# Kernel optimization log

Measured on AMD Instinct MI355X. Metric: run time of the kernel, lower is better.

Reference implementation:

```python
import jax, jax.numpy as jnp
import numpy as np
import math

EMBED_DIM = 1024
N_HEADS = 16
HEAD_DIM = EMBED_DIM // N_HEADS
NUM_FEATURES = 32
R_NODES = 2
EPS = 1e-06
C_CONST = 2.0 + EPS
CHUNK = 512


def setup_inputs() -> dict:
    key = jax.random.key(0)
    ks = jax.random.split(key, 8)
    B, T = 2, 4096
    x = jax.random.normal(ks[0], (B, T, EMBED_DIM), dtype=jnp.float32)
    w_qkv = jax.random.normal(ks[1], (3 * EMBED_DIM, EMBED_DIM), dtype=jnp.float32) * 0.02
    b_qkv = jnp.zeros((3 * EMBED_DIM,), dtype=jnp.float32)
    w_out = jax.random.normal(ks[2], (EMBED_DIM, EMBED_DIM), dtype=jnp.float32) * 0.02
    b_out = jnp.zeros((EMBED_DIM,), dtype=jnp.float32)
    omega = jax.random.normal(ks[3], (R_NODES, N_HEADS, HEAD_DIM, NUM_FEATURES), dtype=jnp.float32)
    nodes, weights = np.polynomial.laguerre.laggauss(R_NODES)
    quad_nodes = jnp.asarray(nodes, dtype=jnp.float32) / C_CONST
    quad_weights = jnp.asarray(weights, dtype=jnp.float32) / C_CONST
    return {"x": x, "w_qkv": w_qkv, "b_qkv": b_qkv, "w_out": w_out,
            "b_out": b_out, "omega": omega, "quad_nodes": quad_nodes,
            "quad_weights": quad_weights}


def _compute_features(z, omega, quad_nodes, quad_weights):
    # z: [B,H,T,D] -> fused features [B,H,T,R*M]
    R, M = omega.shape[0], omega.shape[-1]
    nrm = jnp.linalg.norm(z, axis=-1, keepdims=True)
    zn = z / jnp.maximum(nrm, 1e-12)  # F.normalize
    proj = jnp.einsum('bhtd,rhdm->rbhtm', zn, omega)
    inv_sqrt_m = 1.0 / math.sqrt(M)
    poly = (proj ** 2) * inv_sqrt_m
    s = quad_nodes.reshape(R, 1, 1, 1, 1)
    sqrt_2s = jnp.sqrt(2.0 * jnp.maximum(quad_nodes, 0.0)).reshape(R, 1, 1, 1, 1)
    exp_arg = jnp.clip(proj * sqrt_2s - s, -20.0, 20.0)
    prf = jnp.exp(exp_arg) * inv_sqrt_m
    sqw = jnp.sqrt(jnp.maximum(quad_weights, 0.0)).reshape(R, 1, 1, 1, 1)
    fused = poly * prf * sqw  # [R,B,H,T,M]
    B, H, T = z.shape[0], z.shape[1], z.shape[2]
    return jnp.transpose(fused, (1, 2, 3, 0, 4)).reshape(B, H, T, R * M)


def _forward(x, w_qkv, b_qkv, w_out, b_out, omega, quad_nodes, quad_weights):
    B, T, C = x.shape
    H, D = N_HEADS, HEAD_DIM
    qkv = x @ w_qkv.T + b_qkv  # [B,T,3C]
    q, k, v = jnp.split(qkv, 3, axis=-1)
    def to_bhtd(t):
        return jnp.transpose(t.reshape(B, T, H, D), (0, 2, 1, 3)).astype(jnp.float32)
    q, k, v = to_bhtd(q), to_bhtd(k), to_bhtd(v)
    qf = _compute_features(q, omega, quad_nodes, quad_weights)  # [B,H,T,F]
    kf = _compute_features(k, omega, quad_nodes, quad_weights)
    F_dim = qf.shape[-1]
    nc = T // CHUNK
    # chunked causal linear attention via scan over chunks
    def to_chunks(t):  # [B,H,T,...] -> [nc,B,H,CHUNK,...]
        new_shape = (t.shape[0], t.shape[1], nc, CHUNK) + t.shape[3:]
        return jnp.moveaxis(t.reshape(new_shape), 2, 0)
    qf_c, kf_c, v_c = to_chunks(qf), to_chunks(kf), to_chunks(v)

    kv0 = jnp.zeros((B, H, F_dim, D), dtype=jnp.float32)
    k0 = jnp.zeros((B, H, F_dim), dtype=jnp.float32)

    def step(carry, inp):
        kv_s, k_s = carry
        qc, kc, vc = inp
        kv_prod = jnp.einsum('bhtf,bhtd->bhtfd', kc, vc)
        kv_cum = jnp.cumsum(kv_prod, axis=2) + kv_s[:, :, None]
        k_cum = jnp.cumsum(kc, axis=2) + k_s[:, :, None]
        ctx = jnp.einsum('bhtf,bhtfd->bhtd', qc, kv_cum)
        den = jnp.maximum(jnp.einsum('bhtf,bhtf->bht', qc, k_cum), 1e-06)
        out_c = ctx / den[..., None]
        return (kv_cum[:, :, -1], k_cum[:, :, -1]), out_c

    _, out_chunks = jax.lax.scan(step, (kv0, k0), (qf_c, kf_c, v_c))
    out = jnp.moveaxis(out_chunks, 0, 2).reshape(B, H, T, D)  # [B,H,T,D]
    out = jnp.transpose(out, (0, 2, 1, 3)).reshape(B, T, C)
    return out @ w_out.T + b_out


def reference(x, w_qkv, b_qkv, w_out, b_out, omega, quad_nodes, quad_weights):
    return _forward(x, w_qkv, b_qkv, w_out, b_out, omega, quad_nodes, quad_weights)
```

## Files before the change

kernel.cpp:

```cpp
#include <hip/hip_runtime.h>
#include <math.h>

#define EMBED   1024
#define THREEC  3072
#define NH      16
#define HD      64
#define NFEAT   64
#define RN      2
#define MM_     32
#define B_      2
#define T_      4096
#define L_      64
#define NC_     64
#define BH_     32

typedef __attribute__((ext_vector_type(8))) short bf16x8;
typedef __attribute__((ext_vector_type(4))) float f32x4;

__device__ __forceinline__ float bf2f(short s) {
    unsigned u = ((unsigned)(unsigned short)s) << 16;
    return __builtin_bit_cast(float, u);
}
__device__ __forceinline__ short f2bf(float f) {
    unsigned u = __builtin_bit_cast(unsigned, f);
    u += 0x7fff + ((u >> 16) & 1);
    return (short)(u >> 16);
}
__device__ __forceinline__ void gload16(const short* g, short* l) {
    __builtin_amdgcn_global_load_lds(
        (const __attribute__((address_space(1))) void*)g,
        (__attribute__((address_space(3))) void*)l, 16, 0, 0);
}

__global__ __launch_bounds__(256) void cast_kernel(
    const float* __restrict__ in, short* __restrict__ out, int n8)
{
    int i = blockIdx.x * 256 + threadIdx.x;
    if (i >= n8) return;
    const float4* p = (const float4*)in + (size_t)i * 2;
    float4 a = p[0], b = p[1];
    bf16x8 o = { f2bf(a.x), f2bf(a.y), f2bf(a.z), f2bf(a.w),
                 f2bf(b.x), f2bf(b.y), f2bf(b.z), f2bf(b.w) };
    *((bf16x8*)out + i) = o;
}

__global__ __launch_bounds__(256) void omega_prep(
    const float* __restrict__ omega, short* __restrict__ hi, short* __restrict__ lo)
{
    int i = blockIdx.x * 256 + threadIdx.x;
    if (i >= NH * NFEAT * HD) return;
    int d = i & 63;
    int f = (i >> 6) & 63;
    int h = i >> 12;
    int r = f >> 5, m = f & 31;
    float w = omega[(((size_t)(r * NH + h) * HD + d) * MM_) + m];
    short a = f2bf(w);
    hi[i] = a;
    lo[i] = f2bf(w - bf2f(a));
}

template<int OUTBF>
__global__ __launch_bounds__(256) void gemm_bf16(
    const short* __restrict__ A,
    const short* __restrict__ W,
    const float* __restrict__ bias,
    float* __restrict__ Cf, short* __restrict__ Cb,
    int M, int N, int K)
{
    __shared__ short lA[2][128 * 32];
    __shared__ short lB[2][128 * 32];
    const int tid  = threadIdx.x;
    const int bm   = blockIdx.y * 128;
    const int bn   = blockIdx.x * 128;
    const int lane = tid & 63;
    const int wave = tid >> 6;
    const int row0 = (wave >> 1) * 64;
    const int col0 = (wave & 1) * 64;
    const int lr   = lane & 15;
    const int kg8  = (lane >> 4) * 8;

    f32x4 acc[4][4] = {};

#define STAGE(buf, k0)                                                        \
    {                                                                         \
        _Pragma("unroll")                                                     \
        for (int i = 0; i < 2; ++i) {                                         \
            int idx = i * 256 + tid;                                          \
            int row = idx >> 2, kq = (idx & 3) * 8;                           \
            gload16(&A[(size_t)(bm + row) * K + (k0) + kq], &lA[buf][idx * 8]); \
            gload16(&W[(size_t)(bn + row) * K + (k0) + kq], &lB[buf][idx * 8]); \
        }                                                                     \
    }

    const int KT = K >> 5;
    STAGE(0, 0);
    __syncthreads();
    int cur = 0;
    for (int kt = 0; kt < KT; ++kt) {
        if (kt + 1 < KT) STAGE(cur ^ 1, (kt + 1) * 32);
        const short* As = lA[cur];
        const short* Bs = lB[cur];
        bf16x8 af[4], bfr[4];
        #pragma unroll
        for (int m = 0; m < 4; ++m)
            af[m] = *(const bf16x8*)&As[(row0 + m * 16 + lr) * 32 + kg8];
        #pragma unroll
        for (int n = 0; n < 4; ++n)
            bfr[n] = *(const bf16x8*)&Bs[(col0 + n * 16 + lr) * 32 + kg8];
        #pragma unroll
        for (int m = 0; m < 4; ++m)
            #pragma unroll
            for (int n = 0; n < 4; ++n)
                acc[m][n] = __builtin_amdgcn_mfma_f32_16x16x32_bf16(
                    af[m], bfr[n], acc[m][n], 0, 0, 0);
        __syncthreads();
        cur ^= 1;
    }
#undef STAGE

    #pragma unroll
    for (int n = 0; n < 4; ++n) {
        const int col = bn + col0 + n * 16 + (lane & 15);
        const float bv = bias[col];
        #pragma unroll
        for (int m = 0; m < 4; ++m) {
            const int rbase = bm + row0 + m * 16 + (lane >> 4) * 4;
            #pragma unroll
            for (int j = 0; j < 4; ++j) {
                const float v = acc[m][n][j] + bv;
                if (OUTBF) Cb[(size_t)(rbase + j) * N + col] = f2bf(v);
                else       Cf[(size_t)(rbase + j) * N + col] = v;
            }
        }
    }
}

__global__ __launch_bounds__(256) void features_mfma(
    const short* __restrict__ qkvb,
    const short* __restrict__ omgH,
    const short* __restrict__ omgL,
    const float* __restrict__ qn,
    const float* __restrict__ qw,
    short* __restrict__ qf,
    short* __restrict__ kf)
{
    __shared__ short zq[64][72];
    __shared__ short zk[64][72];
    __shared__ short omh[64][72];
    __shared__ short oml[64][72];
    __shared__ float invn[2][64];

    const int tid = threadIdx.x;
    const int bh  = blockIdx.x >> 6;
    const int tb  = blockIdx.x & 63;
    const int b   = bh >> 4, h = bh & 15;
    const int t0  = tb * 64;

    {
        const int row = tid >> 2;
        const int c0  = (tid & 3) * 16;
        const size_t zbase = ((size_t)(b * T_ + t0 + row)) * THREEC + h * HD + c0;
        const size_t obase = ((size_t)h * NFEAT + row) * HD + c0;
        *(bf16x8*)&zq[row][c0]      = *(const bf16x8*)&qkvb[zbase];
        *(bf16x8*)&zq[row][c0 + 8]  = *(const bf16x8*)&qkvb[zbase + 8];
        *(bf16x8*)&zk[row][c0]      = *(const bf16x8*)&qkvb[zbase + EMBED];
        *(bf16x8*)&zk[row][c0 + 8]  = *(const bf16x8*)&qkvb[zbase + EMBED + 8];
        *(bf16x8*)&omh[row][c0]     = *(const bf16x8*)&omgH[obase];
        *(bf16x8*)&omh[row][c0 + 8] = *(const bf16x8*)&omgH[obase + 8];
        *(bf16x8*)&oml[row][c0]     = *(const bf16x8*)&omgL[obase];
        *(bf16x8*)&oml[row][c0 + 8] = *(const bf16x8*)&omgL[obase + 8];
    }
    __syncthreads();

    {
        const int t = tid >> 2;
        const int q = tid & 3;
        #pragma unroll
        for (int p = 0; p < 2; ++p) {
            const short* Z = p ? &zk[t][q * 16] : &zq[t][q * 16];
            float ss = 0.0f;
            #pragma unroll
            for (int j = 0; j < 16; ++j) { float v = bf2f(Z[j]); ss += v * v; }
            ss += __shfl_xor(ss, 1, 64);
            ss += __shfl_xor(ss, 2, 64);
            if (q == 0) invn[p][t] = 1.0f / fmaxf(sqrtf(ss), 1e-12f);
        }
    }
    __syncthreads();

    const int wave = tid >> 6;
    const int lane = tid & 63;
    const int p    = wave >> 1;
    const int half = wave & 1;
    const short (*Z)[72] = p ? zk : zq;

    const float s0 = qn[0], s1 = qn[1];
    const float sq2s0 = sqrtf(2.0f * fmaxf(s0, 0.0f));
    const float sq2s1 = sqrtf(2.0f * fmaxf(s1, 0.0f));
    const float sc0 = sqrtf(fmaxf(qw[0], 0.0f)) * (1.0f / 32.0f);
    const float sc1 = sqrtf(fmaxf(qw[1], 0.0f)) * (1.0f / 32.0f);

    const int lr  = lane & 15;
    const int kg8 = (lane >> 4) * 8;

    f32x4 acc[2][4] = {};
    #pragma unroll
    for (int kk = 0; kk < 2; ++kk) {
        bf16x8 a[2], bh8[4], bl8[4];
        #pragma unroll
        for (int m = 0; m < 2; ++m)
            a[m] = *(const bf16x8*)&Z[half * 32 + m * 16 + lr][kk * 32 + kg8];
        #pragma unroll
        for (int n = 0; n < 4; ++n) {
            bh8[n] = *(const bf16x8*)&omh[n * 16 + lr][kk * 32 + kg8];
            bl8[n] = *(const bf16x8*)&oml[n * 16 + lr][kk * 32 + kg8];
        }
        #pragma unroll
        for (int m = 0; m < 2; ++m)
            #pragma unroll
            for (int n = 0; n < 4; ++n) {
                acc[m][n] = __builtin_amdgcn_mfma_f32_16x16x32_bf16(
                    a[m], bh8[n], acc[m][n], 0, 0, 0);
                acc[m][n] = __builtin_amdgcn_mfma_f32_16x16x32_bf16(
                    a[m], bl8[n], acc[m][n], 0, 0, 0);
            }
    }

    short* dstbase = (p ? kf : qf) + ((size_t)bh * T_ + t0) * NFEAT;
    #pragma unroll
    for (int n = 0; n < 4; ++n) {
        const int f = n * 16 + (lane & 15);
        const float s_r   = (n < 2) ? s0 : s1;
        const float sq2s  = (n < 2) ? sq2s0 : sq2s1;
        const float scale = (n < 2) ? sc0 : sc1;
        #pragma unroll
        for (int m = 0; m < 2; ++m) {
            const int tb4 = half * 32 + m * 16 + (lane >> 4) * 4;
            #pragma unroll
            for (int j = 0; j < 4; ++j) {
                const int t = tb4 + j;
                const float proj = acc[m][n][j] * invn[p][t];
                const float arg = fminf(fmaxf(proj * sq2s - s_r, -20.0f), 20.0f);
                const float val = proj * proj * __expf(arg) * scale;
                dstbase[(size_t)t * NFEAT + f] = f2bf(val);
            }
        }
    }
}

__global__ __launch_bounds__(256) void chunk_sums(
    const short* __restrict__ kf,
    const short* __restrict__ qkvb,
    float* __restrict__ cKV,
    float* __restrict__ cK)
{
    __shared__ float kfs[64][64];
    __shared__ float vs[64][64];
    float (*st)[65] = (float(*)[65])kfs;

    const int tid = threadIdx.x;
    const int chunk = blockIdx.x;
    const int bh = chunk >> 6, c = chunk & 63;
    const int b = bh >> 4, h = bh & 15;
    const int t0 = c * L_;

    {
        const int row = tid >> 2;
        const int c0  = (tid & 3) * 16;
        const short* krow = kf + ((size_t)bh * T_ + t0 + row) * NFEAT;
        const short* vrow = qkvb + ((size_t)(b * T_ + t0 + row)) * THREEC + 2 * EMBED + h * HD;
        bf16x8 k0 = *(const bf16x8*)&krow[c0], k1 = *(const bf16x8*)&krow[c0 + 8];
        bf16x8 v0 = *(const bf16x8*)&vrow[c0], v1 = *(const bf16x8*)&vrow[c0 + 8];
        #pragma unroll
        for (int j = 0; j < 8; ++j) {
            kfs[row][c0 + j]     = bf2f(k0[j]);
            kfs[row][c0 + 8 + j] = bf2f(k1[j]);
            vs[row][c0 + j]      = bf2f(v0[j]);
            vs[row][c0 + 8 + j]  = bf2f(v1[j]);
        }
    }
    __syncthreads();

    const int f  = tid >> 2;
    const int d0 = (tid & 3) * 16;
    float acc[16] = {};
    float ks = 0.0f;
    for (int t = 0; t < L_; ++t) {
        const float kft = kfs[t][f];
        ks += kft;
        #pragma unroll
        for (int j = 0; j < 16; ++j) acc[j] += kft * vs[t][d0 + j];
    }
    if ((tid & 3) == 0) cK[(size_t)chunk * NFEAT + f] = ks;
    __syncthreads();

    #pragma unroll
    for (int j = 0; j < 16; ++j) st[f][d0 + j] = acc[j];
    __syncthreads();

    {
        const int d  = tid >> 2;
        const int f0 = (tid & 3) * 16;
        float* dst = cKV + (size_t)chunk * (NFEAT * HD) + tid * 16;
        #pragma unroll
        for (int q = 0; q < 4; ++q) {
            float4 o;
            o.x = st[f0 + q * 4 + 0][d];
            o.y = st[f0 + q * 4 + 1][d];
            o.z = st[f0 + q * 4 + 2][d];
            o.w = st[f0 + q * 4 + 3][d];
            *(float4*)&dst[q * 4] = o;
        }
    }
}

__global__ __launch_bounds__(256) void prefix_scan(
    float* __restrict__ cKV, float* __restrict__ cK)
{
    const int bh  = blockIdx.x >> 2;
    const int sl  = blockIdx.x & 3;
    const int tid = threadIdx.x;
    float4* base = (float4*)(cKV + (size_t)bh * NC_ * (NFEAT * HD) + sl * 1024) + tid;
    float4 n0 = base[0];
    float4 n1 = base[1024];
    float4 pref; pref.x = pref.y = pref.z = pref.w = 0.0f;
    for (int c = 0; c < NC_; ++c) {
        float4 cur = n0;
        n0 = n1;
        if (c + 2 < NC_) n1 = base[(size_t)(c + 2) * 1024];
        else { n1.x = n1.y = n1.z = n1.w = 0.0f; }
        base[(size_t)c * 1024] = pref;
        pref.x += cur.x; pref.y += cur.y; pref.z += cur.z; pref.w += cur.w;
    }
    if (sl == 0 && tid < 64) {
        float* kb = cK + (size_t)bh * NC_ * NFEAT + tid;
        float m0 = kb[0];
        float m1 = kb[64];
        float p = 0.0f;
        for (int c = 0; c < NC_; ++c) {
            float cu = m0;
            m0 = m1;
            m1 = (c + 2 < NC_) ? kb[(size_t)(c + 2) * 64] : 0.0f;
            kb[(size_t)c * 64] = p;
            p += cu;
        }
    }
}

__global__ __launch_bounds__(256) void intra_mfma(
    const short* __restrict__ qf,
    const short* __restrict__ kf,
    const short* __restrict__ qkvb,
    const float* __restrict__ cKV,
    const float* __restrict__ cK,
    short* __restrict__ attnb)
{
    __shared__ short Qs[64][72];
    __shared__ short Ks[64][72];
    __shared__ short Vt[64][72];
    __shared__ short Pp[64][72];
    __shared__ short At[64][72];
    __shared__ float rs_l[64], qkp_l[64], cKp[64];

    const int tid = threadIdx.x;
    const int chunk = blockIdx.x;
    const int bh = chunk >> 6, c = chunk & 63;
    const int b = bh >> 4, h = bh & 15;
    const int t0 = c * L_;

    {
        const int row = tid >> 2;
        const int c0  = (tid & 3) * 16;
        const short* qrow = qf + ((size_t)bh * T_ + t0 + row) * NFEAT;
        const short* krow = kf + ((size_t)bh * T_ + t0 + row) * NFEAT;
        const short* vrow = qkvb + ((size_t)(b * T_ + t0 + row)) * THREEC + 2 * EMBED + h * HD;
        *(bf16x8*)&Qs[row][c0]     = *(const bf16x8*)&qrow[c0];
        *(bf16x8*)&Qs[row][c0 + 8] = *(const bf16x8*)&qrow[c0 + 8];
        *(bf16x8*)&Ks[row][c0]     = *(const bf16x8*)&krow[c0];
        *(bf16x8*)&Ks[row][c0 + 8] = *(const bf16x8*)&krow[c0 + 8];
        bf16x8 v0 = *(const bf16x8*)&vrow[c0], v1 = *(const bf16x8*)&vrow[c0 + 8];
        #pragma unroll
        for (int j = 0; j < 8; ++j) {
            Vt[c0 + j][row]     = v0[j];
            Vt[c0 + 8 + j][row] = v1[j];
        }
        const float* pbase = cKV + (size_t)chunk * (NFEAT * HD) + tid * 16;
        float4 p0 = *(const float4*)&pbase[0],  p1 = *(const float4*)&pbase[4];
        float4 p2 = *(const float4*)&pbase[8],  p3 = *(const float4*)&pbase[12];
        bf16x8 o0 = { f2bf(p0.x), f2bf(p0.y), f2bf(p0.z), f2bf(p0.w),
                      f2bf(p1.x), f2bf(p1.y), f2bf(p1.z), f2bf(p1.w) };
        bf16x8 o1 = { f2bf(p2.x), f2bf(p2.y), f2bf(p2.z), f2bf(p2.w),
                      f2bf(p3.x), f2bf(p3.y), f2bf(p3.z), f2bf(p3.w) };
        *(bf16x8*)&Pp[row][c0]     = o0;
        *(bf16x8*)&Pp[row][c0 + 8] = o1;
        if (tid < 64) cKp[tid] = cK[(size_t)chunk * NFEAT + tid];
    }
    __syncthreads();

    const int wave = tid >> 6;
    const int lane = tid & 63;
    const int lr   = lane & 15;
    const int kg   = (lane >> 4) * 8;
    const int r0   = wave * 16;

    bf16x8 aq[2];
    aq[0] = *(const bf16x8*)&Qs[r0 + lr][kg];
    aq[1] = *(const bf16x8*)&Qs[r0 + lr][32 + kg];
    f32x4 accA[4] = {};
    #pragma unroll
    for (int n = 0; n < 4; ++n) {
        accA[n] = __builtin_amdgcn_mfma_f32_16x16x32_bf16(
            aq[0], *(const bf16x8*)&Ks[n * 16 + lr][kg], accA[n], 0, 0, 0);
        accA[n] = __builtin_amdgcn_mfma_f32_16x16x32_bf16(
            aq[1], *(const bf16x8*)&Ks[n * 16 + lr][32 + kg], accA[n], 0, 0, 0);
    }
    float rsum[4] = {0.0f, 0.0f, 0.0f, 0.0f};
    #pragma unroll
    for (int n = 0; n < 4; ++n) {
        const int s = n * 16 + lr;
        #pragma unroll
        for (int j = 0; j < 4; ++j) {
            const int t = r0 + (lane >> 4) * 4 + j;
            const float a = (s <= t) ? accA[n][j] : 0.0f;
            rsum[j] += a;
            At[t][s] = f2bf(a);
        }
    }
    #pragma unroll
    for (int j = 0; j < 4; ++j) {
        rsum[j] += __shfl_xor(rsum[j], 1, 64);
        rsum[j] += __shfl_xor(rsum[j], 2, 64);
        rsum[j] += __shfl_xor(rsum[j], 4, 64);
        rsum[j] += __shfl_xor(rsum[j], 8, 64);
    }
    if (lr == 0) {
        #pragma unroll
        for (int j = 0; j < 4; ++j) rs_l[r0 + (lane >> 4) * 4 + j] = rsum[j];
    }

    {
        const int t  = tid >> 2;
        const int fq = (tid & 3) * 16;
        float s = 0.0f;
        #pragma unroll
        for (int j = 0; j < 16; ++j) s += bf2f(Qs[t][fq + j]) * cKp[fq + j];
        s += __shfl_xor(s, 1, 64);
        s += __shfl_xor(s, 2, 64);
        if ((tid & 3) == 0) qkp_l[t] = s;
    }
    __syncthreads();

    bf16x8 aa[2];
    aa[0] = *(const bf16x8*)&At[r0 + lr][kg];
    aa[1] = *(const bf16x8*)&At[r0 + lr][32 + kg];
    f32x4 acc[4] = {};
    #pragma unroll
    for (int n = 0; n < 4; ++n) {
        acc[n] = __builtin_amdgcn_mfma_f32_16x16x32_bf16(
            aa[0], *(const bf16x8*)&Vt[n * 16 + lr][kg], acc[n], 0, 0, 0);
        acc[n] = __builtin_amdgcn_mfma_f32_16x16x32_bf16(
            aa[1], *(const bf16x8*)&Vt[n * 16 + lr][32 + kg], acc[n], 0, 0, 0);
        acc[n] = __builtin_amdgcn_mfma_f32_16x16x32_bf16(
            aq[0], *(const bf16x8*)&Pp[n * 16 + lr][kg], acc[n], 0, 0, 0);
        acc[n] = __builtin_amdgcn_mfma_f32_16x16x32_bf16(
            aq[1], *(const bf16x8*)&Pp[n * 16 + lr][32 + kg], acc[n], 0, 0, 0);
    }

    float inv[4];
    #pragma unroll
    for (int j = 0; j < 4; ++j) {
        const int t = r0 + (lane >> 4) * 4 + j;
        inv[j] = 1.0f / fmaxf(rs_l[t] + qkp_l[t], 1e-6f);
    }
    #pragma unroll
    for (int n = 0; n < 4; ++n) {
        const int d = n * 16 + lr;
        #pragma unroll
        for (int j = 0; j < 4; ++j) {
            const int t = r0 + (lane >> 4) * 4 + j;
            attnb[((size_t)(b * T_ + t0 + t)) * EMBED + h * HD + d] =
                f2bf(acc[n][j] * inv[j]);
        }
    }
}

extern "C" void kernel_launch(void* const* d_in, const int* in_sizes, int n_in,
                              void* d_out, int out_size, void* d_ws, size_t ws_size,
                              hipStream_t stream)
{
    const float* x     = (const float*)d_in[0];
    const float* w_qkv = (const float*)d_in[1];
    const float* b_qkv = (const float*)d_in[2];
    const float* w_out = (const float*)d_in[3];
    const float* b_out = (const float*)d_in[4];
    const float* omega = (const float*)d_in[5];
    const float* qn    = (const float*)d_in[6];
    const float* qw    = (const float*)d_in[7];
    float* out = (float*)d_out;

    short* xb    = (short*)d_ws;
    short* wqb   = xb    + 8388608;
    short* wob   = wqb   + 3145728;
    short* qkvb  = wob   + 1048576;
    short* attnb = qkvb  + 25165824;
    short* omgH  = attnb + 8388608;
    short* omgL  = omgH  + 65536;
    short* qfb   = omgL  + 65536;
    short* kfb   = qfb   + 8388608;
    float* cKV   = (float*)(kfb + 8388608);
    float* cK    = cKV + 8388608;

    const int M = B_ * T_;

    cast_kernel<<<dim3(8388608 / 8 / 256), 256, 0, stream>>>(x, xb, 8388608 / 8);
    cast_kernel<<<dim3(3145728 / 8 / 256), 256, 0, stream>>>(w_qkv, wqb, 3145728 / 8);
    cast_kernel<<<dim3(1048576 / 8 / 256), 256, 0, stream>>>(w_out, wob, 1048576 / 8);
    omega_prep<<<dim3(256), 256, 0, stream>>>(omega, omgH, omgL);

    gemm_bf16<1><<<dim3(THREEC / 128, M / 128), 256, 0, stream>>>(
        xb, wqb, b_qkv, nullptr, qkvb, M, THREEC, EMBED);
    features_mfma<<<dim3(BH_ * (T_ / 64)), 256, 0, stream>>>(
        qkvb, omgH, omgL, qn, qw, qfb, kfb);
    chunk_sums<<<dim3(BH_ * NC_), 256, 0, stream>>>(kfb, qkvb, cKV, cK);
    prefix_scan<<<dim3(BH_ * 4), 256, 0, stream>>>(cKV, cK);
    intra_mfma<<<dim3(BH_ * NC_), 256, 0, stream>>>(qfb, kfb, qkvb, cKV, cK, attnb);
    gemm_bf16<0><<<dim3(EMBED / 128, M / 128), 256, 0, stream>>>(
        attnb, wob, b_out, out, nullptr, M, EMBED, EMBED);
}
```

Baseline: 194.4 us.

## Replace QKV GEMM with 256x256 four-stage pipelined MFMA kernel

Adds a new bf16 GEMM for the QKV projection that uses 256x256 tiles, 512 threads, a 4-buffer LDS ring fed by async global-to-LDS loads, and double-buffered register fragments. MFMA work for the current k-tile is interleaved with LDS reads and global staging for later tiles, with priority hints and an XCD-aware block swizzle. The aim is to hide memory latency and raise MFMA utilization on the largest GEMM. In exchange the kernel uses 128 KB of LDS and many registers per block, which limits occupancy and assumes dimensions divisible by 256 and an even k-tile count.

```diff
diff --git a/kernel.cpp b/kernel.cpp
--- a/kernel.cpp
+++ b/kernel.cpp
@@ -57,6 +57,129 @@
     short a = f2bf(w);
     hi[i] = a;
     lo[i] = f2bf(w - bf2f(a));
+}
+
+__device__ __forceinline__ bf16x8 lds_frag(const short* base, int row, int G) {
+    const int off = row * 32 + ((G ^ (row & 3)) << 3);
+    return *(const bf16x8*)(base + off);
+}
+
+__global__ __launch_bounds__(512, 2) void gemm_pipe256(
+    const short* __restrict__ A,
+    const short* __restrict__ W,
+    const float* __restrict__ bias,
+    short* __restrict__ Cb,
+    int M, int N, int K)
+{
+    __shared__ short lA[4][256 * 32];
+    __shared__ short lB[4][256 * 32];
+
+    const int tid  = threadIdx.x;
+    const int nbn  = N >> 8;
+    const int nwg  = gridDim.x;
+    const int cpx  = nwg >> 3;
+    const int bid  = blockIdx.x;
+    const int swz  = (bid & 7) * cpx + (bid >> 3);
+    const int bm   = (swz / nbn) << 8;
+    const int bn   = (swz % nbn) << 8;
+
+    const int lane = tid & 63;
+    const int wid  = tid >> 6;
+    const int wm   = wid >> 2;
+    const int wn   = wid & 3;
+    const int lr   = lane & 15;
+    const int G    = lane >> 4;
+
+    const int r2   = tid >> 2;
+    const int gs   = (tid & 3) ^ (r2 & 3);
+    const int KT   = K >> 5;
+
+    auto stageA = [&](int buf, int kt) {
+        const int k0 = kt << 5;
+        gload16(&A[(size_t)(bm + r2) * K + k0 + gs * 8],       &lA[buf][tid * 8]);
+        gload16(&A[(size_t)(bm + 128 + r2) * K + k0 + gs * 8], &lA[buf][4096 + tid * 8]);
+    };
+    auto stageB = [&](int buf, int kt) {
+        const int k0 = kt << 5;
+        gload16(&W[(size_t)(bn + r2) * K + k0 + gs * 8],       &lB[buf][tid * 8]);
+        gload16(&W[(size_t)(bn + 128 + r2) * K + k0 + gs * 8], &lB[buf][4096 + tid * 8]);
+    };
+
+    f32x4 acc[8][4] = {};
+    bf16x8 ra0[8], rb0[4], ra1[8], rb1[4];
+
+#define DS_READ_A(dst, bufidx, frlo)                                          \
+    _Pragma("unroll")                                                         \
+    for (int fr = (frlo); fr < (frlo) + 4; ++fr)                              \
+        dst[fr] = lds_frag(&lA[bufidx][0], wm * 128 + fr * 16 + lr, G);
+#define DS_READ_B(dst, bufidx, fclo)                                          \
+    _Pragma("unroll")                                                         \
+    for (int fc = (fclo); fc < (fclo) + 2; ++fc)                              \
+        dst[fc] = lds_frag(&lB[bufidx][0], wn * 64 + fc * 16 + lr, G);
+#define MFMA_HALF(RA, RB, frlo)                                               \
+    _Pragma("unroll")                                                         \
+    for (int fr = (frlo); fr < (frlo) + 4; ++fr)                              \
+        _Pragma("unroll")                                                     \
+        for (int fc = 0; fc < 4; ++fc)                                        \
+            acc[fr][fc] = __builtin_amdgcn_mfma_f32_16x16x32_bf16(            \
+                RA[fr], RB[fc], acc[fr][fc], 0, 0, 0);
+
+#define KTILE_BODY(kt, RA_CUR, RB_CUR, RA_NXT, RB_NXT)                        \
+    {                                                                         \
+        const int bstg = ((kt) + 3) & 3;                                      \
+        const int bnxt = ((kt) + 1) & 3;                                      \
+        if ((kt) + 2 < KT) asm volatile("s_waitcnt vmcnt(4)" ::: "memory");   \
+        else               asm volatile("s_waitcnt vmcnt(0)" ::: "memory");   \
+        __builtin_amdgcn_s_barrier();                                         \
+        __builtin_amdgcn_sched_barrier(0);                                    \
+        if ((kt) + 1 < KT) { DS_READ_A(RA_NXT, bnxt, 0)                       \
+                             DS_READ_B(RB_NXT, bnxt, 0) }                     \
+        if ((kt) + 3 < KT) stageA(bstg, (kt) + 3);                            \
+        __builtin_amdgcn_s_setprio(1);                                        \
+        MFMA_HALF(RA_CUR, RB_CUR, 0)                                          \
+        __builtin_amdgcn_s_setprio(0);                                        \
+        __builtin_amdgcn_sched_barrier(0);                                    \
+        if ((kt) + 1 < KT) { DS_READ_A(RA_NXT, bnxt, 4)                       \
+                             DS_READ_B(RB_NXT, bnxt, 2) }                     \
+        if ((kt) + 3 < KT) stageB(bstg, (kt) + 3);                            \
+        __builtin_amdgcn_s_setprio(1);                                        \
+        MFMA_HALF(RA_CUR, RB_CUR, 4)                                          \
+        __builtin_amdgcn_s_setprio(0);                                        \
+        __builtin_amdgcn_sched_barrier(0);                                    \
+    }
+
+    stageA(0, 0); stageB(0, 0);
+    stageA(1, 1); stageB(1, 1);
+    stageA(2, 2); stageB(2, 2);
+    asm volatile("s_waitcnt vmcnt(8)" ::: "memory");
+    __builtin_amdgcn_s_barrier();
+    __builtin_amdgcn_sched_barrier(0);
+    DS_READ_A(ra0, 0, 0) DS_READ_A(ra0, 0, 4)
+    DS_READ_B(rb0, 0, 0) DS_READ_B(rb0, 0, 2)
+
+    const int KT2 = KT >> 1;
+    for (int kti = 0; kti < KT2; ++kti) {
+        const int kt = kti * 2;
+        KTILE_BODY(kt,     ra0, rb0, ra1, rb1)
+        KTILE_BODY(kt + 1, ra1, rb1, ra0, rb0)
+    }
+#undef DS_READ_A
+#undef DS_READ_B
+#undef MFMA_HALF
+#undef KTILE_BODY
+
+    #pragma unroll
+    for (int fc = 0; fc < 4; ++fc) {
+        const int col = bn + wn * 64 + fc * 16 + lr;
+        const float bv = bias[col];
+        #pragma unroll
+        for (int fr = 0; fr < 8; ++fr) {
+            const int rbase = bm + wm * 128 + fr * 16 + G * 4;
+            #pragma unroll
+            for (int j = 0; j < 4; ++j)
+                Cb[(size_t)(rbase + j) * N + col] = f2bf(acc[fr][fc][j] + bv);
+        }
+    }
 }
 
 template<int OUTBF>
@@ -517,8 +640,8 @@
     cast_kernel<<<dim3(1048576 / 8 / 256), 256, 0, stream>>>(w_out, wob, 1048576 / 8);
     omega_prep<<<dim3(256), 256, 0, stream>>>(omega, omgH, omgL);
 
-    gemm_bf16<1><<<dim3(THREEC / 128, M / 128), 256, 0, stream>>>(
-        xb, wqb, b_qkv, nullptr, qkvb, M, THREEC, EMBED);
+    gemm_pipe256<<<dim3((M / 256) * (THREEC / 256)), 512, 0, stream>>>(
+        xb, wqb, b_qkv, qkvb, M, THREEC, EMBED);
     features_mfma<<<dim3(BH_ * (T_ / 64)), 256, 0, stream>>>(
         qkvb, omgH, omgL, qn, qw, qfb, kfb);
     chunk_sums<<<dim3(BH_ * NC_), 256, 0, stream>>>(kfb, qkvb, cKV, cK);
```

New measurement: 196.2 us. Within noise of the previous version (+0.9%).

## Replace QKV projection GEMM with 256x256 eight-phase pipelined bf16 kernel

Applied to the files above, without the earlier changes.

Adds a new bf16 MFMA GEMM for the QKV projection with 256x256 tiles, 512 threads, direct global-to-LDS loads, XOR-swizzled LDS layout, and an eight-phase ping-pong schedule that interleaves loads, LDS reads and MFMAs under explicit waitcnt/barriers and s_setprio. It also swizzles block order across XCDs and stages the output through LDS for coalesced 16-byte stores. The aim is to raise MFMA utilization and cut global memory stalls in the largest GEMM, at the cost of 128KB LDS per block and fragile hand-tuned synchronization.

```diff
diff --git a/kernel.cpp b/kernel.cpp
--- a/kernel.cpp
+++ b/kernel.cpp
@@ -59,6 +59,178 @@
     lo[i] = f2bf(w - bf2f(a));
 }
 
+__global__ __launch_bounds__(512, 2) void gemm_8ph(
+    const short* __restrict__ Ag,
+    const short* __restrict__ Wg,
+    const float* __restrict__ bias,
+    short* __restrict__ Cb,
+    int M, int N, int K)
+{
+    __shared__ short LDS[65536];
+
+    const int tid  = threadIdx.x;
+    const int nbn  = N >> 8;
+    const int nwg  = gridDim.x;
+    const int cpx  = nwg >> 3;
+    const int bid  = blockIdx.x;
+    const int swz  = (bid & 7) * cpx + (bid >> 3);
+    const int bm   = (swz / nbn) << 8;
+    const int bn   = (swz % nbn) << 8;
+
+    const int lane = tid & 63;
+    const int wid  = tid >> 6;
+    const int wm   = wid >> 2;
+    const int wn   = wid & 3;
+    const int lr   = lane & 15;
+    const int G    = lane >> 4;
+
+    const int r2   = tid >> 2;
+    const int gsw  = (tid & 3) ^ ((r2 >> 1) & 3);
+    const int KT   = K >> 6;
+    const int KT2  = KT >> 1;
+
+    f32x4  acc[8][4] = {};
+    bf16x8 afk0[8], afk1[8], bfk0[4], bfk1[4];
+    {
+        bf16x8 z = {0,0,0,0,0,0,0,0};
+        #pragma unroll
+        for (int i = 0; i < 8; ++i) afk1[i] = z;
+        #pragma unroll
+        for (int i = 0; i < 4; ++i) bfk1[i] = z;
+    }
+
+#define ST_A(buf, kh, kt) { \
+        short* ldst = &LDS[((buf) * 2 + (kh)) * 8192]; \
+        gload16(&Ag[(size_t)(bm + r2) * K + (kt) * 64 + (kh) * 32 + gsw * 8], \
+                ldst + tid * 8); \
+        gload16(&Ag[(size_t)(bm + 128 + r2) * K + (kt) * 64 + (kh) * 32 + gsw * 8], \
+                ldst + 4096 + tid * 8); }
+#define ST_B(buf, kh, kt) { \
+        short* ldst = &LDS[32768 + ((buf) * 2 + (kh)) * 8192]; \
+        gload16(&Wg[(size_t)(bn + r2) * K + (kt) * 64 + (kh) * 32 + gsw * 8], \
+                ldst + tid * 8); \
+        gload16(&Wg[(size_t)(bn + 128 + r2) * K + (kt) * 64 + (kh) * 32 + gsw * 8], \
+                ldst + 4096 + tid * 8); }
+#define RD_A(dst, buf, kh) { \
+        const short* lsrc = &LDS[((buf) * 2 + (kh)) * 8192]; \
+        _Pragma("unroll") \
+        for (int fr = 0; fr < 8; ++fr) { \
+            const int row = wm * 128 + fr * 16 + lr; \
+            dst[fr] = *(const bf16x8*)&lsrc[row * 32 + ((G ^ ((row >> 1) & 3)) << 3)]; } }
+#define RD_B(dst, buf, kh) { \
+        const short* lsrc = &LDS[32768 + ((buf) * 2 + (kh)) * 8192]; \
+        _Pragma("unroll") \
+        for (int fc = 0; fc < 4; ++fc) { \
+            const int row = wn * 64 + fc * 16 + lr; \
+            dst[fc] = *(const bf16x8*)&lsrc[row * 32 + ((G ^ ((row >> 1) & 3)) << 3)]; } }
+#define MM(frh, AF, BF) \
+        _Pragma("unroll") \
+        for (int fr = 0; fr < 4; ++fr) \
+            _Pragma("unroll") \
+            for (int fc = 0; fc < 4; ++fc) \
+                acc[(frh) * 4 + fr][fc] = __builtin_amdgcn_mfma_f32_16x16x32_bf16( \
+                    AF[(frh) * 4 + fr], BF[fc], acc[(frh) * 4 + fr][fc], 0, 0, 0);
+#define BAR   __builtin_amdgcn_s_barrier()
+#define LGKM0 { asm volatile("s_waitcnt lgkmcnt(0)" ::: "memory"); \
+                __builtin_amdgcn_sched_barrier(0); }
+#define PRIO1 __builtin_amdgcn_s_setprio(1)
+#define PRIO0 __builtin_amdgcn_s_setprio(0)
+
+    ST_A(0, 0, 0); ST_B(0, 0, 0); ST_A(0, 1, 0); ST_B(0, 1, 0);
+    ST_A(1, 0, 1); ST_B(1, 0, 1); ST_A(1, 1, 1);
+    asm volatile("s_waitcnt vmcnt(6)" ::: "memory");
+    BAR;
+
+    for (int t = 0; t < KT2; ++t) {
+        const int ktA = 2 * t;
+        const int ktB = 2 * t + 1;
+        RD_A(afk0, 0, 0);
+        ST_B(1, 1, ktB);
+        BAR; LGKM0;
+        PRIO1; MM(1, afk1, bfk1); PRIO0;
+        BAR;
+        RD_B(bfk0, 0, 0);
+        if (ktA + 2 < KT) ST_A(0, 0, ktA + 2);
+        BAR; LGKM0;
+        PRIO1; MM(0, afk0, bfk0); PRIO0;
+        BAR;
+        RD_A(afk1, 0, 1);
+        if (ktA + 2 < KT) ST_B(0, 0, ktA + 2);
+        BAR; LGKM0;
+        PRIO1; MM(1, afk0, bfk0); PRIO0;
+        BAR;
+        RD_B(bfk1, 0, 1);
+        if (ktA + 2 < KT) ST_A(0, 1, ktA + 2);
+        BAR; LGKM0;
+        PRIO1; MM(0, afk1, bfk1); PRIO0;
+        if (ktA + 2 < KT) { asm volatile("s_waitcnt vmcnt(6)" ::: "memory"); }
+        else              { asm volatile("s_waitcnt vmcnt(0)" ::: "memory"); }
+        BAR;
+        RD_A(afk0, 1, 0);
+        if (ktA + 2 < KT) ST_B(0, 1, ktA + 2);
+        BAR; LGKM0;
+        PRIO1; MM(1, afk1, bfk1); PRIO0;
+        BAR;
+        RD_B(bfk0, 1, 0);
+        if (ktB + 2 < KT) ST_A(1, 0, ktB + 2);
+        BAR; LGKM0;
+        PRIO1; MM(0, afk0, bfk0); PRIO0;
+        BAR;
+        RD_A(afk1, 1, 1);
+        if (ktB + 2 < KT) ST_B(1, 0, ktB + 2);
+        BAR; LGKM0;
+        PRIO1; MM(1, afk0, bfk0); PRIO0;
+        BAR;
+        RD_B(bfk1, 1, 1);
+        if (ktB + 2 < KT) ST_A(1, 1, ktB + 2);
+        BAR; LGKM0;
+        PRIO1; MM(0, afk1, bfk1); PRIO0;
+        if (ktB + 2 < KT) { asm volatile("s_waitcnt vmcnt(6)" ::: "memory"); }
+        else              { asm volatile("s_waitcnt vmcnt(0)" ::: "memory"); }
+        BAR;
+    }
+    MM(1, afk1, bfk1);
+
+#undef ST_A
+#undef ST_B
+#undef RD_A
+#undef RD_B
+#undef MM
+
+    float bv[4];
+    #pragma unroll
+    for (int fc = 0; fc < 4; ++fc)
+        bv[fc] = bias[bn + wn * 64 + fc * 16 + lr];
+
+    short* E = (short*)LDS;
+    #pragma unroll 1
+    for (int pass = 0; pass < 2; ++pass) {
+        __syncthreads();
+        if (wm == pass) {
+            #pragma unroll
+            for (int fr = 0; fr < 8; ++fr)
+                #pragma unroll
+                for (int fc = 0; fc < 4; ++fc) {
+                    const int col = wn * 64 + fc * 16 + lr;
+                    #pragma unroll
+                    for (int j = 0; j < 4; ++j) {
+                        const int rl = fr * 16 + G * 4 + j;
+                        E[rl * 264 + col] = f2bf(acc[fr][fc][j] + bv[fc]);
+                    }
+                }
+        }
+        __syncthreads();
+        #pragma unroll
+        for (int i = 0; i < 8; ++i) {
+            const int idx = i * 512 + tid;
+            const int rl  = idx >> 5;
+            const int c8  = idx & 31;
+            bf16x8 v = *(const bf16x8*)&E[rl * 264 + c8 * 8];
+            *(bf16x8*)&Cb[(size_t)(bm + pass * 128 + rl) * N + bn + c8 * 8] = v;
+        }
+    }
+}
+
 template<int OUTBF>
 __global__ __launch_bounds__(256) void gemm_bf16(
     const short* __restrict__ A,
@@ -121,13 +293,13 @@
     #pragma unroll
     for (int n = 0; n < 4; ++n) {
         const int col = bn + col0 + n * 16 + (lane & 15);
-        const float bv = bias[col];
+        const float bvv = bias[col];
         #pragma unroll
         for (int m = 0; m < 4; ++m) {
             const int rbase = bm + row0 + m * 16 + (lane >> 4) * 4;
             #pragma unroll
             for (int j = 0; j < 4; ++j) {
-                const float v = acc[m][n][j] + bv;
+                const float v = acc[m][n][j] + bvv;
                 if (OUTBF) Cb[(size_t)(rbase + j) * N + col] = f2bf(v);
                 else       Cf[(size_t)(rbase + j) * N + col] = v;
             }
@@ -517,8 +689,8 @@
     cast_kernel<<<dim3(1048576 / 8 / 256), 256, 0, stream>>>(w_out, wob, 1048576 / 8);
     omega_prep<<<dim3(256), 256, 0, stream>>>(omega, omgH, omgL);
 
-    gemm_bf16<1><<<dim3(THREEC / 128, M / 128), 256, 0, stream>>>(
-        xb, wqb, b_qkv, nullptr, qkvb, M, THREEC, EMBED);
+    gemm_8ph<<<dim3((M / 256) * (THREEC / 256)), 512, 0, stream>>>(
+        xb, wqb, b_qkv, qkvb, M, THREEC, EMBED);
     features_mfma<<<dim3(BH_ * (T_ / 64)), 256, 0, stream>>>(
         qkvb, omgH, omgL, qn, qw, qfb, kfb);
     chunk_sums<<<dim3(BH_ * NC_), 256, 0, stream>>>(kfb, qkvb, cKV, cK);
```

Result: slower. 242.8 us (+24.9%).

## Fuse cast kernels and merge chunk sums into feature kernel via MFMA

Applied to the files above, without the earlier changes.

The three fp32-to-bf16 cast launches and the omega split are merged into one prep kernel. The chunk_sums kernel is folded into the feature kernel: the key features are also written transposed into LDS, the V chunk is transposed into LDS, and the per-chunk K^T V is computed with bf16 MFMA instead of a scalar fp32 loop. This removes three launches and one re-read of kf and V from global memory. In exchange the per-chunk KV sums are now built from bf16 operands rather than fp32 values.

```diff
diff --git a/kernel.cpp b/kernel.cpp
--- a/kernel.cpp
+++ b/kernel.cpp
@@ -32,31 +32,40 @@
         (__attribute__((address_space(3))) void*)l, 16, 0, 0);
 }
 
-__global__ __launch_bounds__(256) void cast_kernel(
-    const float* __restrict__ in, short* __restrict__ out, int n8)
+#define NV_X   1048576
+#define NV_WQ  393216
+#define NV_WO  131072
+#define NV_ALL (NV_X + NV_WQ + NV_WO)
+__global__ __launch_bounds__(256) void prep_kernel(
+    const float* __restrict__ x, const float* __restrict__ wq,
+    const float* __restrict__ wo, const float* __restrict__ omega,
+    short* __restrict__ xb, short* __restrict__ wqb, short* __restrict__ wob,
+    short* __restrict__ omgH, short* __restrict__ omgL)
 {
     int i = blockIdx.x * 256 + threadIdx.x;
-    if (i >= n8) return;
-    const float4* p = (const float4*)in + (size_t)i * 2;
-    float4 a = p[0], b = p[1];
-    bf16x8 o = { f2bf(a.x), f2bf(a.y), f2bf(a.z), f2bf(a.w),
-                 f2bf(b.x), f2bf(b.y), f2bf(b.z), f2bf(b.w) };
-    *((bf16x8*)out + i) = o;
-}
-
-__global__ __launch_bounds__(256) void omega_prep(
-    const float* __restrict__ omega, short* __restrict__ hi, short* __restrict__ lo)
-{
-    int i = blockIdx.x * 256 + threadIdx.x;
-    if (i >= NH * NFEAT * HD) return;
-    int d = i & 63;
-    int f = (i >> 6) & 63;
-    int h = i >> 12;
-    int r = f >> 5, m = f & 31;
-    float w = omega[(((size_t)(r * NH + h) * HD + d) * MM_) + m];
-    short a = f2bf(w);
-    hi[i] = a;
-    lo[i] = f2bf(w - bf2f(a));
+    if (i < NV_ALL) {
+        const float* src; short* dst; int k;
+        if (i < NV_X)            { src = x;  dst = xb;  k = i; }
+        else if (i < NV_X+NV_WQ) { src = wq; dst = wqb; k = i - NV_X; }
+        else                     { src = wo; dst = wob; k = i - NV_X - NV_WQ; }
+        const float4* p = (const float4*)src + (size_t)k * 2;
+        float4 a = p[0], b = p[1];
+        bf16x8 o = { f2bf(a.x), f2bf(a.y), f2bf(a.z), f2bf(a.w),
+                     f2bf(b.x), f2bf(b.y), f2bf(b.z), f2bf(b.w) };
+        *((bf16x8*)dst + k) = o;
+    } else {
+        int j = i - NV_ALL;
+        if (j < NH * NFEAT * HD) {
+            int d = j & 63;
+            int f = (j >> 6) & 63;
+            int h = j >> 12;
+            int r = f >> 5, m = f & 31;
+            float w = omega[(((size_t)(r * NH + h) * HD + d) * MM_) + m];
+            short a = f2bf(w);
+            omgH[j] = a;
+            omgL[j] = f2bf(w - bf2f(a));
+        }
+    }
 }
 
 template<int OUTBF>
@@ -121,13 +130,13 @@
     #pragma unroll
     for (int n = 0; n < 4; ++n) {
         const int col = bn + col0 + n * 16 + (lane & 15);
-        const float bv = bias[col];
+        const float bvv = bias[col];
         #pragma unroll
         for (int m = 0; m < 4; ++m) {
             const int rbase = bm + row0 + m * 16 + (lane >> 4) * 4;
             #pragma unroll
             for (int j = 0; j < 4; ++j) {
-                const float v = acc[m][n][j] + bv;
+                const float v = acc[m][n][j] + bvv;
                 if (OUTBF) Cb[(size_t)(rbase + j) * N + col] = f2bf(v);
                 else       Cf[(size_t)(rbase + j) * N + col] = v;
             }
@@ -135,14 +144,16 @@
     }
 }
 
-__global__ __launch_bounds__(256) void features_mfma(
+__global__ __launch_bounds__(256) void features_chunk(
     const short* __restrict__ qkvb,
     const short* __restrict__ omgH,
     const short* __restrict__ omgL,
     const float* __restrict__ qn,
     const float* __restrict__ qw,
     short* __restrict__ qf,
-    short* __restrict__ kf)
+    short* __restrict__ kf,
+    float* __restrict__ cKV,
+    float* __restrict__ cK)
 {
     __shared__ short zq[64][72];
     __shared__ short zk[64][72];
@@ -150,11 +161,12 @@
     __shared__ short oml[64][72];
     __shared__ float invn[2][64];
 
-    const int tid = threadIdx.x;
-    const int bh  = blockIdx.x >> 6;
-    const int tb  = blockIdx.x & 63;
-    const int b   = bh >> 4, h = bh & 15;
-    const int t0  = tb * 64;
+    const int tid   = threadIdx.x;
+    const int chunk = blockIdx.x;
+    const int bh    = chunk >> 6;
+    const int c     = chunk & 63;
+    const int b     = bh >> 4, h = bh & 15;
+    const int t0    = c * 64;
 
     {
         const int row = tid >> 2;
@@ -201,7 +213,8 @@
     const float sc1 = sqrtf(fmaxf(qw[1], 0.0f)) * (1.0f / 32.0f);
 
     const int lr  = lane & 15;
-    const int kg8 = (lane >> 4) * 8;
+    const int G   = lane >> 4;
+    const int kg8 = G * 8;
 
     f32x4 acc[2][4] = {};
     #pragma unroll
@@ -225,92 +238,79 @@
                     a[m], bl8[n], acc[m][n], 0, 0, 0);
             }
     }
-
-    short* dstbase = (p ? kf : qf) + ((size_t)bh * T_ + t0) * NFEAT;
-    #pragma unroll
-    for (int n = 0; n < 4; ++n) {
-        const int f = n * 16 + (lane & 15);
-        const float s_r   = (n < 2) ? s0 : s1;
-        const float sq2s  = (n < 2) ? sq2s0 : sq2s1;
-        const float scale = (n < 2) ? sc0 : sc1;
-        #pragma unroll
-        for (int m = 0; m < 2; ++m) {
-            const int tb4 = half * 32 + m * 16 + (lane >> 4) * 4;
+    __syncthreads();
+
+    short (*kfT)[72] = zq;
+    short (*vT)[72]  = zk;
+    {
+        short* dstbase = (p ? kf : qf) + ((size_t)bh * T_ + t0) * NFEAT;
+        #pragma unroll
+        for (int n = 0; n < 4; ++n) {
+            const int f = n * 16 + lr;
+            const float s_r   = (n < 2) ? s0 : s1;
+            const float sq2s  = (n < 2) ? sq2s0 : sq2s1;
+            const float scale = (n < 2) ? sc0 : sc1;
             #pragma unroll
-            for (int j = 0; j < 4; ++j) {
-                const int t = tb4 + j;
-                const float proj = acc[m][n][j] * invn[p][t];
-                const float arg = fminf(fmaxf(proj * sq2s - s_r, -20.0f), 20.0f);
-                const float val = proj * proj * __expf(arg) * scale;
-                dstbase[(size_t)t * NFEAT + f] = f2bf(val);
+            for (int m = 0; m < 2; ++m) {
+                const int tb4 = half * 32 + m * 16 + G * 4;
+                #pragma unroll
+                for (int j = 0; j < 4; ++j) {
+                    const int t = tb4 + j;
+                    const float proj = acc[m][n][j] * invn[p][t];
+                    const float arg = fminf(fmaxf(proj * sq2s - s_r, -20.0f), 20.0f);
+                    const float val = proj * proj * __expf(arg) * scale;
+                    const short vb  = f2bf(val);
+                    dstbase[(size_t)t * NFEAT + f] = vb;
+                    if (p == 1) kfT[f][t] = vb;
+                }
             }
         }
     }
-}
-
-__global__ __launch_bounds__(256) void chunk_sums(
-    const short* __restrict__ kf,
-    const short* __restrict__ qkvb,
-    float* __restrict__ cKV,
-    float* __restrict__ cK)
-{
-    __shared__ float kfs[64][64];
-    __shared__ float vs[64][64];
-    float (*st)[65] = (float(*)[65])kfs;
-
-    const int tid = threadIdx.x;
-    const int chunk = blockIdx.x;
-    const int bh = chunk >> 6, c = chunk & 63;
-    const int b = bh >> 4, h = bh & 15;
-    const int t0 = c * L_;
-
     {
         const int row = tid >> 2;
         const int c0  = (tid & 3) * 16;
-        const short* krow = kf + ((size_t)bh * T_ + t0 + row) * NFEAT;
-        const short* vrow = qkvb + ((size_t)(b * T_ + t0 + row)) * THREEC + 2 * EMBED + h * HD;
-        bf16x8 k0 = *(const bf16x8*)&krow[c0], k1 = *(const bf16x8*)&krow[c0 + 8];
+        const short* vrow = qkvb + ((size_t)(b * T_ + t0 + row)) * THREEC
+                          + 2 * EMBED + h * HD;
         bf16x8 v0 = *(const bf16x8*)&vrow[c0], v1 = *(const bf16x8*)&vrow[c0 + 8];
         #pragma unroll
         for (int j = 0; j < 8; ++j) {
-            kfs[row][c0 + j]     = bf2f(k0[j]);
-            kfs[row][c0 + 8 + j] = bf2f(k1[j]);
-            vs[row][c0 + j]      = bf2f(v0[j]);
-            vs[row][c0 + 8 + j]  = bf2f(v1[j]);
-        }
-    }
-    __syncthreads();
-
-    const int f  = tid >> 2;
-    const int d0 = (tid & 3) * 16;
-    float acc[16] = {};
-    float ks = 0.0f;
-    for (int t = 0; t < L_; ++t) {
-        const float kft = kfs[t][f];
-        ks += kft;
-        #pragma unroll
-        for (int j = 0; j < 16; ++j) acc[j] += kft * vs[t][d0 + j];
-    }
-    if ((tid & 3) == 0) cK[(size_t)chunk * NFEAT + f] = ks;
-    __syncthreads();
-
-    #pragma unroll
-    for (int j = 0; j < 16; ++j) st[f][d0 + j] = acc[j];
-    __syncthreads();
-
-    {
-        const int d  = tid >> 2;
-        const int f0 = (tid & 3) * 16;
-        float* dst = cKV + (size_t)chunk * (NFEAT * HD) + tid * 16;
-        #pragma unroll
-        for (int q = 0; q < 4; ++q) {
-            float4 o;
-            o.x = st[f0 + q * 4 + 0][d];
-            o.y = st[f0 + q * 4 + 1][d];
-            o.z = st[f0 + q * 4 + 2][d];
-            o.w = st[f0 + q * 4 + 3][d];
-            *(float4*)&dst[q * 4] = o;
-        }
+            vT[c0 + j][row]     = v0[j];
+            vT[c0 + 8 + j][row] = v1[j];
+        }
+    }
+    __syncthreads();
+
+    {
+        bf16x8 a2[2], bv8[4][2];
+        a2[0] = *(const bf16x8*)&kfT[wave * 16 + lr][kg8];
+        a2[1] = *(const bf16x8*)&kfT[wave * 16 + lr][32 + kg8];
+        #pragma unroll
+        for (int n = 0; n < 4; ++n) {
+            bv8[n][0] = *(const bf16x8*)&vT[n * 16 + lr][kg8];
+            bv8[n][1] = *(const bf16x8*)&vT[n * 16 + lr][32 + kg8];
+        }
+        f32x4 sa[4] = {};
+        #pragma unroll
+        for (int n = 0; n < 4; ++n) {
+            sa[n] = __builtin_amdgcn_mfma_f32_16x16x32_bf16(a2[0], bv8[n][0], sa[n], 0, 0, 0);
+            sa[n] = __builtin_amdgcn_mfma_f32_16x16x32_bf16(a2[1], bv8[n][1], sa[n], 0, 0, 0);
+        }
+        float* base = cKV + (size_t)chunk * (NFEAT * HD);
+        #pragma unroll
+        for (int n = 0; n < 4; ++n) {
+            float4 o; o.x = sa[n][0]; o.y = sa[n][1]; o.z = sa[n][2]; o.w = sa[n][3];
+            *(float4*)&base[(n * 16 + lr) * NFEAT + wave * 16 + G * 4] = o;
+        }
+    }
+    {
+        const int f  = tid >> 2;
+        const int tq = tid & 3;
+        float s = 0.0f;
+        #pragma unroll
+        for (int j = 0; j < 16; ++j) s += bf2f(kfT[f][tq * 16 + j]);
+        s += __shfl_xor(s, 1, 64);
+        s += __shfl_xor(s, 2, 64);
+        if (tq == 0) cK[(size_t)chunk * NFEAT + f] = s;
     }
 }
 
@@ -512,16 +512,13 @@
 
     const int M = B_ * T_;
 
-    cast_kernel<<<dim3(8388608 / 8 / 256), 256, 0, stream>>>(x, xb, 8388608 / 8);
-    cast_kernel<<<dim3(3145728 / 8 / 256), 256, 0, stream>>>(w_qkv, wqb, 3145728 / 8);
-    cast_kernel<<<dim3(1048576 / 8 / 256), 256, 0, stream>>>(w_out, wob, 1048576 / 8);
-    omega_prep<<<dim3(256), 256, 0, stream>>>(omega, omgH, omgL);
+    prep_kernel<<<dim3((NV_ALL + 65536) / 256), 256, 0, stream>>>(
+        x, w_qkv, w_out, omega, xb, wqb, wob, omgH, omgL);
 
     gemm_bf16<1><<<dim3(THREEC / 128, M / 128), 256, 0, stream>>>(
         xb, wqb, b_qkv, nullptr, qkvb, M, THREEC, EMBED);
-    features_mfma<<<dim3(BH_ * (T_ / 64)), 256, 0, stream>>>(
-        qkvb, omgH, omgL, qn, qw, qfb, kfb);
-    chunk_sums<<<dim3(BH_ * NC_), 256, 0, stream>>>(kfb, qkvb, cKV, cK);
+    features_chunk<<<dim3(BH_ * NC_), 256, 0, stream>>>(
+        qkvb, omgH, omgL, qn, qw, qfb, kfb, cKV, cK);
     prefix_scan<<<dim3(BH_ * 4), 256, 0, stream>>>(cKV, cK);
     intra_mfma<<<dim3(BH_ * NC_), 256, 0, stream>>>(qfb, kfb, qkvb, cKV, cK, attnb);
     gemm_bf16<0><<<dim3(EMBED / 128, M / 128), 256, 0, stream>>>(
```

New measurement: 170.7 us. 1.14x faster.
